# Kernel optimization log

Measured on AMD Instinct MI355X. Metric: run time of the kernel, lower is better.

Reference implementation:

```python
import jax, jax.numpy as jnp
import numpy as np

C = 256
NUM_HEADS = 4
NBLK = 6  # 3 stages x depth 2
WS = (2, 8, 8)   # 3D window
SS = (1, 4, 4)   # shift for odd blocks
N_WIN = WS[0] * WS[1] * WS[2]  # 128 tokens per window
RPB_SIZE = (2 * WS[0] - 1) * (2 * WS[1] - 1) * (2 * WS[2] - 1)  # 675


def _rel_index():
    coords = np.stack(np.meshgrid(np.arange(WS[0]), np.arange(WS[1]), np.arange(WS[2]), indexing='ij'))
    coords = coords.reshape(3, -1)
    rel = (coords[:, :, None] - coords[:, None, :]).transpose(1, 2, 0)
    rel[:, :, 0] += WS[0] - 1
    rel[:, :, 1] += WS[1] - 1
    rel[:, :, 2] += WS[2] - 1
    rel[:, :, 0] *= (2 * WS[1] - 1) * (2 * WS[2] - 1)
    rel[:, :, 1] *= (2 * WS[2] - 1)
    return jnp.asarray(rel.sum(-1))  # [N_WIN, N_WIN]

REL_IDX = _rel_index()


def window_partition(x):
    # [B,D,H,W,C] -> [B*nW, N_WIN, C]
    B, D, H, W, Cc = x.shape
    x = x.reshape(B, D // WS[0], WS[0], H // WS[1], WS[1], W // WS[2], WS[2], Cc)
    return x.transpose(0, 1, 3, 5, 2, 4, 6, 7).reshape(-1, N_WIN, Cc)


def window_reverse(win, B, D, H, W):
    Cc = win.shape[-1]
    x = win.reshape(B, D // WS[0], H // WS[1], W // WS[2], WS[0], WS[1], WS[2], Cc)
    return x.transpose(0, 1, 4, 2, 5, 3, 6, 7).reshape(B, D, H, W, Cc)


def attn_mask(D, H, W):
    # standard shifted-window mask, computed on host constants
    img = np.zeros((1, D, H, W, 1), np.float32)
    cnt = 0
    for d in (slice(0, -WS[0]), slice(-WS[0], -SS[0]), slice(-SS[0], None)):
        for h in (slice(0, -WS[1]), slice(-WS[1], -SS[1]), slice(-SS[1], None)):
            for w in (slice(0, -WS[2]), slice(-WS[2], -SS[2]), slice(-SS[2], None)):
                img[:, d, h, w, :] = cnt
                cnt += 1
    mw = img.reshape(1, D // WS[0], WS[0], H // WS[1], WS[1], W // WS[2], WS[2], 1)
    mw = mw.transpose(0, 1, 3, 5, 2, 4, 6, 7).reshape(-1, N_WIN)
    diff = mw[:, None, :] - mw[:, :, None]
    return jnp.asarray(np.where(diff != 0, -100.0, 0.0).astype(np.float32))  # [nW,N,N]


def layer_norm(x, g, b):
    mu = x.mean(-1, keepdims=True)
    var = ((x - mu) ** 2).mean(-1, keepdims=True)
    return (x - mu) * jax.lax.rsqrt(var + 1e-5) * g + b


def setup_inputs() -> dict:
    key = jax.random.key(0)
    ks = jax.random.split(key, 10)
    f = jax.random.normal
    s = 0.02
    return dict(
        x=f(ks[0], (2, 2, 2, 4096, C), jnp.float32),
        n1w=jnp.ones((NBLK, C), jnp.float32), n1b=jnp.zeros((NBLK, C), jnp.float32),
        qkv_w=f(ks[1], (NBLK, C, 3 * C), jnp.float32) * s, qkv_b=jnp.zeros((NBLK, 3 * C), jnp.float32),
        rpb=f(ks[2], (NBLK, RPB_SIZE, NUM_HEADS), jnp.float32) * s,
        proj_w=f(ks[3], (NBLK, C, C), jnp.float32) * s, proj_b=jnp.zeros((NBLK, C), jnp.float32),
        n2w=jnp.ones((NBLK, C), jnp.float32), n2b=jnp.zeros((NBLK, C), jnp.float32),
        mlp1_w=f(ks[4], (NBLK, C, 4 * C), jnp.float32) * s, mlp1_b=jnp.zeros((NBLK, 4 * C), jnp.float32),
        mlp2_w=f(ks[5], (NBLK, 4 * C, C), jnp.float32) * s, mlp2_b=jnp.zeros((NBLK, C), jnp.float32),
        exp_v_w=f(ks[6], (C, 2 * C), jnp.float32) * s,
        exp_v_nw=jnp.ones((C,), jnp.float32), exp_v_nb=jnp.zeros((C,), jnp.float32),
        exp_t_w=f(ks[7], (C, 2 * C), jnp.float32) * s,
        exp_t_nw=jnp.ones((C,), jnp.float32), exp_t_nb=jnp.zeros((C,), jnp.float32),
    )


def reference(x, n1w, n1b, qkv_w, qkv_b, rpb, proj_w, proj_b, n2w, n2b,
              mlp1_w, mlp1_b, mlp2_w, mlp2_b,
              exp_v_w, exp_v_nw, exp_v_nb, exp_t_w, exp_t_nw, exp_t_nb):
    B, T, V, L, _ = x.shape
    H = W = int(round(np.sqrt(L)))
    NH = NUM_HEADS
    dh = C // NH

    def block(h, i, D, shifted, mask):
        # h: [B, D, L, C]
        sc = h
        y = layer_norm(h, n1w[i], n1b[i]).reshape(B, D, H, W, C)
        if shifted:
            y = jnp.roll(y, (-SS[0], -SS[1], -SS[2]), axis=(1, 2, 3))
        win = window_partition(y)  # [B*nW, N, C]
        qkv = (win @ qkv_w[i] + qkv_b[i]).reshape(-1, N_WIN, 3, NH, dh)
        q, k, v = jnp.moveaxis(qkv, 2, 0)              # [B*nW, N, NH, dh]
        q = q.transpose(0, 2, 1, 3)
        k = k.transpose(0, 2, 1, 3)
        v = v.transpose(0, 2, 1, 3)                     # [B*nW, NH, N, dh]
        attn = jnp.einsum('whqd,whkd->whqk', q, k) * (dh ** -0.5)
        attn = attn + rpb[i][REL_IDX].transpose(2, 0, 1)[None]
        if mask is not None:
            nW = mask.shape[0]
            attn = attn.reshape(B, nW, NH, N_WIN, N_WIN) + mask[None, :, None]
            attn = attn.reshape(-1, NH, N_WIN, N_WIN)
        attn = jax.nn.softmax(attn, axis=-1)
        out = jnp.einsum('whqk,whkd->whqd', attn, v).transpose(0, 2, 1, 3).reshape(-1, N_WIN, C)
        out = out @ proj_w[i] + proj_b[i]
        y = window_reverse(out, B, D, H, W)
        if shifted:
            y = jnp.roll(y, (SS[0], SS[1], SS[2]), axis=(1, 2, 3))
        h = sc + y.reshape(B, D, L, C)
        z = layer_norm(h, n2w[i], n2b[i])
        z = jax.nn.gelu(z @ mlp1_w[i] + mlp1_b[i], approximate=False) @ mlp2_w[i] + mlp2_b[i]
        return h + z

    def stage(h, i0, D):
        mask = attn_mask(D, H, W)
        h = block(h, i0, D, False, None)
        h = block(h, i0 + 1, D, True, mask)
        return h

    # stage 1: swin over D = T*V
    h = x.reshape(B, T * V, L, C)
    h = stage(h, 0, T * V)
    h = h.reshape(B, T, V, L, C)

    # stage 2: view patch expand (V -> 2V) + swin
    h = (h @ exp_v_w).reshape(B, T, V, L, 2, C).transpose(0, 1, 2, 4, 3, 5).reshape(B, T, 2 * V, L, C)
    h = layer_norm(h, exp_v_nw, exp_v_nb)
    V2 = 2 * V
    h = h.reshape(B, T * V2, L, C)
    h = stage(h, 2, T * V2)
    h = h.reshape(B, T, V2, L, C)

    # stage 3: temporal patch expand (T -> 2T) + swin
    h = (h @ exp_t_w).reshape(B, T, V2, L, 2, C).transpose(0, 1, 4, 2, 3, 5).reshape(B, 2 * T, V2, L, C)
    h = layer_norm(h, exp_t_nw, exp_t_nb)
    T2 = 2 * T
    h = h.reshape(B, T2 * V2, L, C)
    h = stage(h, 4, T2 * V2)
    return h.reshape(B, T2, V2, L, C)
```

## Files before the change

kernel.cpp:

```cpp
#include <hip/hip_runtime.h>

typedef __bf16 bf16x8 __attribute__((ext_vector_type(8)));
typedef float f32x4 __attribute__((ext_vector_type(4)));
typedef unsigned short u16;
typedef unsigned int u32;

__device__ __forceinline__ u16 f2b(float f) {
    union { float f; u32 u; } v; v.f = f;
    u32 r = v.u + 0x7fffu + ((v.u >> 16) & 1u);
    return (u16)(r >> 16);
}
__device__ __forceinline__ float b2f(u16 u) {
    union { u32 u; float f; } v; v.u = ((u32)u) << 16; return v.f;
}

__global__ __launch_bounds__(256) void ln_kernel(
    const float* __restrict__ h, u16* __restrict__ out,
    const float* __restrict__ g, const float* __restrict__ bb,
    int D, int dsh, int shifted, int mode)
{
    const int lane = threadIdx.x & 63;
    const int t = blockIdx.x * 4 + (threadIdx.x >> 6);
    const float4 xv = *(const float4*)(h + (size_t)t * 256 + lane * 4);
    float s = xv.x + xv.y + xv.z + xv.w;
    float s2 = xv.x*xv.x + xv.y*xv.y + xv.z*xv.z + xv.w*xv.w;
    #pragma unroll
    for (int o = 32; o > 0; o >>= 1) { s += __shfl_xor(s, o); s2 += __shfl_xor(s2, o); }
    const float mu = s * 0.00390625f;
    const float var = s2 * 0.00390625f - mu * mu;
    const float rs = 1.0f / sqrtf(var + 1e-5f);
    const int c0 = lane * 4;
    const float4 gv = *(const float4*)(g + c0);
    const float4 bv = *(const float4*)(bb + c0);
    ushort4 o4;
    o4.x = f2b((xv.x - mu) * rs * gv.x + bv.x);
    o4.y = f2b((xv.y - mu) * rs * gv.y + bv.y);
    o4.z = f2b((xv.z - mu) * rs * gv.z + bv.z);
    o4.w = f2b((xv.w - mu) * rs * gv.w + bv.w);
    size_t oidx;
    if (mode == 1) {
        oidx = (size_t)t * 256 + c0;
    } else {
        const int b = t >> (dsh + 12);
        const int rem = t & ((1 << (dsh + 12)) - 1);
        int d = rem >> 12;
        const int l = rem & 4095;
        int hh = l >> 6, ww = l & 63;
        if (shifted) { d = d ? d - 1 : D - 1; hh = (hh - 4) & 63; ww = (ww - 4) & 63; }
        const int widx = (b << (dsh + 5)) + ((d >> 1) << 6) + ((hh >> 3) << 3) + (ww >> 3);
        const int n = ((d & 1) << 6) + ((hh & 7) << 3) + (ww & 7);
        oidx = ((size_t)(widx * 128 + n)) * 256 + c0;
    }
    *(ushort4*)(out + oidx) = o4;
}

__global__ __launch_bounds__(256) void cast_kernel(const float* __restrict__ in, u16* __restrict__ out, int n4)
{
    const int i = blockIdx.x * 256 + threadIdx.x;
    if (i >= n4) return;
    const float4 v = ((const float4*)in)[i];
    ushort4 o; o.x = f2b(v.x); o.y = f2b(v.y); o.z = f2b(v.z); o.w = f2b(v.w);
    ((ushort4*)out)[i] = o;
}

__global__ __launch_bounds__(256) void wt_kernel(const float* __restrict__ src, u16* __restrict__ dst, int K, int N)
{
    const size_t base = (size_t)blockIdx.y * K * N;
    const int idx = blockIdx.x * 256 + threadIdx.x;
    const int k = idx / N, n = idx - k * N;
    dst[base + (size_t)n * K + k] = f2b(src[base + idx]);
}

struct GemmP {
    const u16* A; const u16* Bt;
    int K;
    const float* bias;
    u16* outb;
    float* outf;
    const float* hin; float* hout;
    int D, shifted, nwsh, row_off;
};

template <int EPI>
__global__ __launch_bounds__(256, 2) void gemm_kernel(GemmP p)
{
    __shared__ __align__(16) u16 As[128 * 40];
    __shared__ __align__(16) u16 Bs[128 * 40];
    const int tid = threadIdx.x;
    const int m0 = blockIdx.x * 128, n0 = blockIdx.y * 128;
    const int K = p.K;
    f32x4 acc[4][4];
    #pragma unroll
    for (int a = 0; a < 4; a++)
        #pragma unroll
        for (int b = 0; b < 4; b++)
            acc[a][b] = f32x4{0.f, 0.f, 0.f, 0.f};

    const int r0 = tid >> 2;
    const int c8 = (tid & 3) * 8;
    const u16* Ag = p.A + (size_t)m0 * K;
    const u16* Bg = p.Bt + (size_t)n0 * K;
    const int lane = tid & 63;
    const int wv = tid >> 6;
    const int wm = (wv & 1) * 64, wn = (wv >> 1) * 64;
    const int l16 = lane & 15, quad = lane >> 4;

    for (int k0 = 0; k0 < K; k0 += 32) {
        const uint4 a0 = *(const uint4*)(Ag + (size_t)r0 * K + k0 + c8);
        const uint4 a1 = *(const uint4*)(Ag + (size_t)(r0 + 64) * K + k0 + c8);
        const uint4 b0 = *(const uint4*)(Bg + (size_t)r0 * K + k0 + c8);
        const uint4 b1 = *(const uint4*)(Bg + (size_t)(r0 + 64) * K + k0 + c8);
        __syncthreads();
        *(uint4*)(As + r0 * 40 + c8) = a0;
        *(uint4*)(As + (r0 + 64) * 40 + c8) = a1;
        *(uint4*)(Bs + r0 * 40 + c8) = b0;
        *(uint4*)(Bs + (r0 + 64) * 40 + c8) = b1;
        __syncthreads();
        bf16x8 af[4], bfr[4];
        #pragma unroll
        for (int mt = 0; mt < 4; mt++) af[mt] = *(const bf16x8*)(As + (wm + mt * 16 + l16) * 40 + quad * 8);
        #pragma unroll
        for (int nt = 0; nt < 4; nt++) bfr[nt] = *(const bf16x8*)(Bs + (wn + nt * 16 + l16) * 40 + quad * 8);
        #pragma unroll
        for (int mt = 0; mt < 4; mt++)
            #pragma unroll
            for (int nt = 0; nt < 4; nt++)
                acc[mt][nt] = __builtin_amdgcn_mfma_f32_16x16x32_bf16(af[mt], bfr[nt], acc[mt][nt], 0, 0, 0);
    }

    #pragma unroll
    for (int mt = 0; mt < 4; mt++) {
        #pragma unroll
        for (int nt = 0; nt < 4; nt++) {
            #pragma unroll
            for (int i = 0; i < 4; i++) {
                const int row = m0 + wm + mt * 16 + quad * 4 + i;
                const int col = n0 + wn + nt * 16 + l16;
                float v = acc[mt][nt][i];
                if constexpr (EPI == 0) {
                    v += p.bias[col];
                    if (col < 256) v *= 0.125f;
                    p.outb[(size_t)row * 768 + col] = f2b(v);
                } else if constexpr (EPI == 1) {
                    v += p.bias[col];
                    const int widx = row >> 7, n = row & 127;
                    const int b = widx >> p.nwsh, rem = widx & ((1 << p.nwsh) - 1);
                    int dd = ((rem >> 6) << 1) + (n >> 6);
                    int hh = (((rem >> 3) & 7) << 3) + ((n >> 3) & 7);
                    int ww = ((rem & 7) << 3) + (n & 7);
                    if (p.shifted) { dd = (dd + 1 == p.D) ? 0 : dd + 1; hh = (hh + 4) & 63; ww = (ww + 4) & 63; }
                    const size_t idx = ((size_t)((b * p.D + dd) * 4096 + hh * 64 + ww)) * 256 + col;
                    p.hout[idx] = p.hin[idx] + v;
                } else if constexpr (EPI == 2) {
                    v += p.bias[col];
                    v = 0.5f * v * (1.0f + erff(v * 0.7071067811865475f));
                    p.outb[(size_t)row * 1024 + col] = f2b(v);
                } else if constexpr (EPI == 3) {
                    v += p.bias[col];
                    const size_t idx = (size_t)(p.row_off + row) * 256 + col;
                    p.hout[idx] = p.hin[idx] + v;
                } else {
                    p.outf[(size_t)row * 512 + col] = v;
                }
            }
        }
    }
}

__global__ __launch_bounds__(256, 2) void attn_mfma_kernel(
    const u16* __restrict__ qkv, u16* __restrict__ att,
    const float* __restrict__ rpbp, int D, int shifted, int w0g, int nwsh)
{
    __shared__ __align__(16) char smem[57856];
    u16* Qs = (u16*)smem;
    u16* Ks = (u16*)(smem + 18432);
    u16* Ps = (u16*)smem;
    u16* Vt = (u16*)(smem + 36864);
    float* rb = (float*)(smem + 54272);
    int* lbl = (int*)(smem + 56972);

    const int wloc = blockIdx.x;
    const int head = blockIdx.y;
    const int tid = threadIdx.x;
    const u16* base = qkv + (size_t)wloc * 98304;

    #pragma unroll
    for (int it = 0; it < 4; it++) {
        const int id = it * 256 + tid;
        const int row = id >> 3, oct = id & 7;
        const size_t ro = (size_t)row * 768 + head * 64 + oct * 8;
        *(uint4*)(Qs + row * 72 + oct * 8) = *(const uint4*)(base + ro);
        *(uint4*)(Ks + row * 72 + oct * 8) = *(const uint4*)(base + ro + 256);
        uint4 vv = *(const uint4*)(base + ro + 512);
        const u16* vp = (const u16*)&vv;
        #pragma unroll
        for (int q = 0; q < 8; q++) Vt[(oct * 8 + q) * 136 + row] = vp[q];
    }
    for (int j = tid; j < 675; j += 256) rb[j] = rpbp[j * 4 + head];
    if (tid < 128) {
        int lv = 0;
        if (shifted) {
            const int widx = w0g + wloc;
            const int rem = widx & ((1 << nwsh) - 1);
            const int d0 = rem >> 6, h0 = (rem >> 3) & 7, w0 = rem & 7;
            const int wd = tid >> 6, wh = (tid >> 3) & 7, ww = tid & 7;
            const int rd = (d0 < (D >> 1) - 1) ? 0 : (1 + wd);
            const int rh = (h0 < 7) ? 0 : (1 + (wh >= 4));
            const int rw = (w0 < 7) ? 0 : (1 + (ww >= 4));
            lv = rd * 9 + rh * 3 + rw;
        }
        lbl[tid] = lv;
    }
    __syncthreads();

    const int wq = tid >> 6;
    const int lane = tid & 63;
    const int l16 = lane & 15, quad = lane >> 4;
    const int myrow0 = wq * 32;

    f32x4 sc[2][8];
    #pragma unroll
    for (int mt = 0; mt < 2; mt++)
        #pragma unroll
        for (int nt = 0; nt < 8; nt++)
            sc[mt][nt] = f32x4{0.f, 0.f, 0.f, 0.f};
    #pragma unroll
    for (int kt = 0; kt < 2; kt++) {
        bf16x8 aq[2];
        #pragma unroll
        for (int mt = 0; mt < 2; mt++)
            aq[mt] = *(const bf16x8*)(Qs + (myrow0 + mt * 16 + l16) * 72 + kt * 32 + quad * 8);
        bf16x8 bk[8];
        #pragma unroll
        for (int nt = 0; nt < 8; nt++)
            bk[nt] = *(const bf16x8*)(Ks + (nt * 16 + l16) * 72 + kt * 32 + quad * 8);
        #pragma unroll
        for (int mt = 0; mt < 2; mt++)
            #pragma unroll
            for (int nt = 0; nt < 8; nt++)
                sc[mt][nt] = __builtin_amdgcn_mfma_f32_16x16x32_bf16(aq[mt], bk[nt], sc[mt][nt], 0, 0, 0);
    }

    float linv[2][4];
    #pragma unroll
    for (int mt = 0; mt < 2; mt++) {
        #pragma unroll
        for (int i = 0; i < 4; i++) {
            const int row = myrow0 + mt * 16 + quad * 4 + i;
            const int rbase = ((row >> 6) + 1) * 225 + (((row >> 3) & 7) + 7) * 15 + ((row & 7) + 7);
            const int lq = lbl[row];
            float mx = -1e30f;
            float sv[8];
            #pragma unroll
            for (int nt = 0; nt < 8; nt++) {
                const int col = nt * 16 + l16;
                float v = sc[mt][nt][i] + rb[rbase - (col >> 6) * 225 - ((col >> 3) & 7) * 15 - (col & 7)];
                if (shifted && lq != lbl[col]) v -= 100.0f;
                sv[nt] = v;
                mx = fmaxf(mx, v);
            }
            #pragma unroll
            for (int o = 1; o < 16; o <<= 1) mx = fmaxf(mx, __shfl_xor(mx, o));
            float l = 0.0f;
            #pragma unroll
            for (int nt = 0; nt < 8; nt++) {
                const float pp = __expf(sv[nt] - mx);
                sc[mt][nt][i] = pp;
                l += pp;
            }
            #pragma unroll
            for (int o = 1; o < 16; o <<= 1) l += __shfl_xor(l, o);
            linv[mt][i] = 1.0f / l;
        }
    }

    __syncthreads();
    #pragma unroll
    for (int mt = 0; mt < 2; mt++)
        #pragma unroll
        for (int nt = 0; nt < 8; nt++)
            #pragma unroll
            for (int i = 0; i < 4; i++)
                Ps[(myrow0 + mt * 16 + quad * 4 + i) * 136 + nt * 16 + l16] = f2b(sc[mt][nt][i]);

    f32x4 oc[2][4];
    #pragma unroll
    for (int mt = 0; mt < 2; mt++)
        #pragma unroll
        for (int nt = 0; nt < 4; nt++)
            oc[mt][nt] = f32x4{0.f, 0.f, 0.f, 0.f};
    #pragma unroll
    for (int kt = 0; kt < 4; kt++) {
        bf16x8 ap[2];
        #pragma unroll
        for (int mt = 0; mt < 2; mt++)
            ap[mt] = *(const bf16x8*)(Ps + (myrow0 + mt * 16 + l16) * 136 + kt * 32 + quad * 8);
        bf16x8 bv[4];
        #pragma unroll
        for (int nt = 0; nt < 4; nt++)
            bv[nt] = *(const bf16x8*)(Vt + (nt * 16 + l16) * 136 + kt * 32 + quad * 8);
        #pragma unroll
        for (int mt = 0; mt < 2; mt++)
            #pragma unroll
            for (int nt = 0; nt < 4; nt++)
                oc[mt][nt] = __builtin_amdgcn_mfma_f32_16x16x32_bf16(ap[mt], bv[nt], oc[mt][nt], 0, 0, 0);
    }

    #pragma unroll
    for (int mt = 0; mt < 2; mt++)
        #pragma unroll
        for (int nt = 0; nt < 4; nt++)
            #pragma unroll
            for (int i = 0; i < 4; i++) {
                const int row = myrow0 + mt * 16 + quad * 4 + i;
                const int col = nt * 16 + l16;
                att[(size_t)(wloc * 128 + row) * 256 + head * 64 + col] = f2b(oc[mt][nt][i] * linv[mt][i]);
            }
}

__global__ __launch_bounds__(256) void expand_ln_kernel(
    const float* __restrict__ sc, float* __restrict__ hout,
    const float* __restrict__ g, const float* __restrict__ bb,
    int it0, int typ)
{
    const int lane = threadIdx.x & 63;
    const int ot = blockIdx.x * 4 + (threadIdx.x >> 6);
    const int itl = ot >> 1, e = ot & 1;
    const float4 xv = *(const float4*)(sc + (size_t)itl * 512 + e * 256 + lane * 4);
    float s = xv.x + xv.y + xv.z + xv.w;
    float s2 = xv.x*xv.x + xv.y*xv.y + xv.z*xv.z + xv.w*xv.w;
    #pragma unroll
    for (int o = 32; o > 0; o >>= 1) { s += __shfl_xor(s, o); s2 += __shfl_xor(s2, o); }
    const float mu = s * 0.00390625f;
    const float var = s2 * 0.00390625f - mu * mu;
    const float rs = 1.0f / sqrtf(var + 1e-5f);
    const int c0 = lane * 4;
    const float4 gv = *(const float4*)(g + c0);
    const float4 bv = *(const float4*)(bb + c0);
    float4 y;
    y.x = (xv.x - mu) * rs * gv.x + bv.x;
    y.y = (xv.y - mu) * rs * gv.y + bv.y;
    y.z = (xv.z - mu) * rs * gv.z + bv.z;
    y.w = (xv.w - mu) * rs * gv.w + bv.w;
    const int it = it0 + itl;
    size_t otg;
    if (typ == 0) {
        const int b = it >> 14, rr = it & 16383;
        const int t = rr >> 13, v = (rr >> 12) & 1, l = rr & 4095;
        otg = (size_t)(((b * 2 + t) * 4 + v * 2 + e) * 4096 + l);
    } else {
        const int b = it >> 15, rr = it & 32767;
        const int t = rr >> 14, v2 = (rr >> 12) & 3, l = rr & 4095;
        otg = (size_t)(((b * 4 + t * 2 + e) * 4 + v2) * 4096 + l);
    }
    *(float4*)(hout + otg * 256 + c0) = y;
}

extern "C" void kernel_launch(void* const* d_in, const int* in_sizes, int n_in,
                              void* d_out, int out_size, void* d_ws, size_t ws_size,
                              hipStream_t stream)
{
    const float* x      = (const float*)d_in[0];
    const float* n1w    = (const float*)d_in[1];
    const float* n1b    = (const float*)d_in[2];
    const float* qkv_w  = (const float*)d_in[3];
    const float* qkv_b  = (const float*)d_in[4];
    const float* rpb    = (const float*)d_in[5];
    const float* proj_w = (const float*)d_in[6];
    const float* proj_b = (const float*)d_in[7];
    const float* n2w    = (const float*)d_in[8];
    const float* n2b    = (const float*)d_in[9];
    const float* mlp1_w = (const float*)d_in[10];
    const float* mlp1_b = (const float*)d_in[11];
    const float* mlp2_w = (const float*)d_in[12];
    const float* mlp2_b = (const float*)d_in[13];
    const float* expv_w = (const float*)d_in[14];
    const float* expv_nw= (const float*)d_in[15];
    const float* expv_nb= (const float*)d_in[16];
    const float* expt_w = (const float*)d_in[17];
    const float* expt_nw= (const float*)d_in[18];
    const float* expt_nb= (const float*)d_in[19];
    (void)in_sizes; (void)n_in; (void)out_size;

    if (ws_size < 352321536ULL) return;

    char* ws = (char*)d_ws;
    float* h    = (float*)ws;
    u16*  winb  = (u16*)(ws + 134217728LL);
    u16*  att   = (u16*)(ws + 134217728LL + 67108864LL);
    char* scr   = ws + 134217728LL + 2LL * 67108864LL;
    u16*  scrb  = (u16*)scr;
    float* scrf = (float*)scr;
    u16* qkvT   = (u16*)(ws + 134217728LL + 3LL * 67108864LL);
    u16* projT  = qkvT + 6 * 768 * 256;
    u16* mlp1T  = projT + 6 * 256 * 256;
    u16* mlp2T  = mlp1T + 6 * 1024 * 256;
    u16* expvT  = mlp2T + 6 * 256 * 1024;
    u16* exptT  = expvT + 512 * 256;

    wt_kernel<<<dim3(768, 6), 256, 0, stream>>>(qkv_w, qkvT, 256, 768);
    wt_kernel<<<dim3(256, 6), 256, 0, stream>>>(proj_w, projT, 256, 256);
    wt_kernel<<<dim3(1024, 6), 256, 0, stream>>>(mlp1_w, mlp1T, 256, 1024);
    wt_kernel<<<dim3(1024, 6), 256, 0, stream>>>(mlp2_w, mlp2T, 1024, 256);
    wt_kernel<<<dim3(512, 1), 256, 0, stream>>>(expv_w, expvT, 256, 512);
    wt_kernel<<<dim3(512, 1), 256, 0, stream>>>(expt_w, exptT, 256, 512);
    hipMemcpyAsync(h, x, 33554432ULL, hipMemcpyDeviceToDevice, stream);

    for (int s = 0; s < 3; s++) {
        const int D = 4 << s;
        const int dsh = 2 + s;
        const int nwsh = dsh + 5;
        const int tokens = 2 * D * 4096;
        const int nch = tokens / 32768;
        for (int j = 0; j < 2; j++) {
            const int i = 2 * s + j;
            ln_kernel<<<dim3(tokens / 4), 256, 0, stream>>>(h, winb, n1w + i * 256, n1b + i * 256, D, dsh, j, 0);
            for (int c = 0; c < nch; c++) {
                GemmP gq{};
                gq.A = winb + (size_t)c * 32768 * 256;
                gq.Bt = qkvT + (size_t)i * 768 * 256;
                gq.K = 256; gq.bias = qkv_b + i * 768; gq.outb = scrb;
                gemm_kernel<0><<<dim3(256, 6), 256, 0, stream>>>(gq);
                attn_mfma_kernel<<<dim3(256, 4), 256, 0, stream>>>(scrb, att + (size_t)c * 32768 * 256,
                                                                   rpb + i * 675 * 4, D, j, c * 256, nwsh);
            }
            GemmP gp{};
            gp.A = att; gp.Bt = projT + (size_t)i * 256 * 256; gp.K = 256;
            gp.bias = proj_b + i * 256; gp.hin = h; gp.hout = h;
            gp.D = D; gp.shifted = j; gp.nwsh = nwsh;
            gemm_kernel<1><<<dim3(tokens / 128, 2), 256, 0, stream>>>(gp);
            ln_kernel<<<dim3(tokens / 4), 256, 0, stream>>>(h, winb, n2w + i * 256, n2b + i * 256, D, dsh, 0, 1);
            for (int c = 0; c < nch; c++) {
                GemmP g1{};
                g1.A = winb + (size_t)c * 32768 * 256;
                g1.Bt = mlp1T + (size_t)i * 1024 * 256;
                g1.K = 256; g1.bias = mlp1_b + i * 1024; g1.outb = scrb;
                gemm_kernel<2><<<dim3(256, 8), 256, 0, stream>>>(g1);
                GemmP g2{};
                g2.A = scrb; g2.Bt = mlp2T + (size_t)i * 256 * 1024; g2.K = 1024;
                g2.bias = mlp2_b + i * 256; g2.hin = h; g2.row_off = c * 32768;
                g2.hout = (s == 2 && j == 1) ? (float*)d_out : h;
                gemm_kernel<3><<<dim3(256, 2), 256, 0, stream>>>(g2);
            }
        }
        if (s < 2) {
            const int ntok = tokens;
            cast_kernel<<<dim3(ntok * 64 / 256), 256, 0, stream>>>(h, winb, ntok * 64);
            const u16* eT = (s == 0) ? expvT : exptT;
            const float* eg = (s == 0) ? expv_nw : expt_nw;
            const float* eb = (s == 0) ? expv_nb : expt_nb;
            for (int c = 0; c < ntok / 32768; c++) {
                GemmP ge{};
                ge.A = winb + (size_t)c * 32768 * 256; ge.Bt = eT; ge.K = 256; ge.outf = scrf;
                gemm_kernel<4><<<dim3(256, 4), 256, 0, stream>>>(ge);
                expand_ln_kernel<<<dim3(16384), 256, 0, stream>>>(scrf, h, eg, eb, c * 32768, s);
            }
        }
    }
}
```

Before: 3.006 ms.

## Use direct global-to-LDS loads with swizzle and stage GEMM epilogue through LDS

The GEMM main loop now uses global_load_lds to copy A/B tiles straight into shared memory, skipping the register round trip. Bank conflicts are avoided with an XOR swizzle instead of a padded stride. The epilogue writes accumulators to an LDS staging buffer in four 32-row chunks so each thread can issue wide vectorized global stores and residual loads instead of scattered scalar ones. This adds extra barriers per chunk and relies on the direct-to-LDS load semantics being correct.

```diff
diff --git a/kernel.cpp b/kernel.cpp
--- a/kernel.cpp
+++ b/kernel.cpp
@@ -12,6 +12,11 @@
 }
 __device__ __forceinline__ float b2f(u16 u) {
     union { u32 u; float f; } v; v.u = ((u32)u) << 16; return v.f;
+}
+__device__ __forceinline__ void gl_lds16(const u16* g, u16* l) {
+    __builtin_amdgcn_global_load_lds(
+        (const __attribute__((address_space(1))) void*)g,
+        (__attribute__((address_space(3))) void*)l, 16, 0, 0);
 }
 
 __global__ __launch_bounds__(256) void ln_kernel(
@@ -84,43 +89,48 @@
 template <int EPI>
 __global__ __launch_bounds__(256, 2) void gemm_kernel(GemmP p)
 {
-    __shared__ __align__(16) u16 As[128 * 40];
-    __shared__ __align__(16) u16 Bs[128 * 40];
+    __shared__ __align__(16) char smem[16896];
+    u16* As = (u16*)smem;
+    u16* Bs = (u16*)(smem + 8192);
+    float* CF = (float*)smem;
+
     const int tid = threadIdx.x;
     const int m0 = blockIdx.x * 128, n0 = blockIdx.y * 128;
     const int K = p.K;
-    f32x4 acc[4][4];
-    #pragma unroll
-    for (int a = 0; a < 4; a++)
-        #pragma unroll
-        for (int b = 0; b < 4; b++)
-            acc[a][b] = f32x4{0.f, 0.f, 0.f, 0.f};
-
-    const int r0 = tid >> 2;
-    const int c8 = (tid & 3) * 8;
-    const u16* Ag = p.A + (size_t)m0 * K;
-    const u16* Bg = p.Bt + (size_t)n0 * K;
     const int lane = tid & 63;
     const int wv = tid >> 6;
     const int wm = (wv & 1) * 64, wn = (wv >> 1) * 64;
     const int l16 = lane & 15, quad = lane >> 4;
 
+    f32x4 acc[4][4];
+    #pragma unroll
+    for (int a = 0; a < 4; a++)
+        #pragma unroll
+        for (int b = 0; b < 4; b++)
+            acc[a][b] = f32x4{0.f, 0.f, 0.f, 0.f};
+
+    const int lrow = lane >> 2;
+    const int c16s = (lane & 3) ^ (lrow & 3);
+    const int rA0 = wv * 16;
+    const u16* Ag = p.A + (size_t)(m0 + rA0 + lrow) * K + c16s * 8;
+    const u16* Bg = p.Bt + (size_t)(n0 + rA0 + lrow) * K + c16s * 8;
+    u16* Al = As + rA0 * 32;
+    u16* Bl = Bs + rA0 * 32;
+    const size_t j64 = (size_t)64 * K;
+    const int fslot = (quad ^ (l16 & 3)) * 8;
+
     for (int k0 = 0; k0 < K; k0 += 32) {
-        const uint4 a0 = *(const uint4*)(Ag + (size_t)r0 * K + k0 + c8);
-        const uint4 a1 = *(const uint4*)(Ag + (size_t)(r0 + 64) * K + k0 + c8);
-        const uint4 b0 = *(const uint4*)(Bg + (size_t)r0 * K + k0 + c8);
-        const uint4 b1 = *(const uint4*)(Bg + (size_t)(r0 + 64) * K + k0 + c8);
         __syncthreads();
-        *(uint4*)(As + r0 * 40 + c8) = a0;
-        *(uint4*)(As + (r0 + 64) * 40 + c8) = a1;
-        *(uint4*)(Bs + r0 * 40 + c8) = b0;
-        *(uint4*)(Bs + (r0 + 64) * 40 + c8) = b1;
+        gl_lds16(Ag + k0, Al);
+        gl_lds16(Ag + j64 + k0, Al + 64 * 32);
+        gl_lds16(Bg + k0, Bl);
+        gl_lds16(Bg + j64 + k0, Bl + 64 * 32);
         __syncthreads();
         bf16x8 af[4], bfr[4];
         #pragma unroll
-        for (int mt = 0; mt < 4; mt++) af[mt] = *(const bf16x8*)(As + (wm + mt * 16 + l16) * 40 + quad * 8);
-        #pragma unroll
-        for (int nt = 0; nt < 4; nt++) bfr[nt] = *(const bf16x8*)(Bs + (wn + nt * 16 + l16) * 40 + quad * 8);
+        for (int mt = 0; mt < 4; mt++) af[mt] = *(const bf16x8*)(As + (wm + mt * 16 + l16) * 32 + fslot);
+        #pragma unroll
+        for (int nt = 0; nt < 4; nt++) bfr[nt] = *(const bf16x8*)(Bs + (wn + nt * 16 + l16) * 32 + fslot);
         #pragma unroll
         for (int mt = 0; mt < 4; mt++)
             #pragma unroll
@@ -128,41 +138,91 @@
                 acc[mt][nt] = __builtin_amdgcn_mfma_f32_16x16x32_bf16(af[mt], bfr[nt], acc[mt][nt], 0, 0, 0);
     }
 
-    #pragma unroll
-    for (int mt = 0; mt < 4; mt++) {
-        #pragma unroll
-        for (int nt = 0; nt < 4; nt++) {
-            #pragma unroll
-            for (int i = 0; i < 4; i++) {
-                const int row = m0 + wm + mt * 16 + quad * 4 + i;
-                const int col = n0 + wn + nt * 16 + l16;
-                float v = acc[mt][nt][i];
-                if constexpr (EPI == 0) {
-                    v += p.bias[col];
-                    if (col < 256) v *= 0.125f;
-                    p.outb[(size_t)row * 768 + col] = f2b(v);
-                } else if constexpr (EPI == 1) {
-                    v += p.bias[col];
-                    const int widx = row >> 7, n = row & 127;
-                    const int b = widx >> p.nwsh, rem = widx & ((1 << p.nwsh) - 1);
-                    int dd = ((rem >> 6) << 1) + (n >> 6);
-                    int hh = (((rem >> 3) & 7) << 3) + ((n >> 3) & 7);
-                    int ww = ((rem & 7) << 3) + (n & 7);
-                    if (p.shifted) { dd = (dd + 1 == p.D) ? 0 : dd + 1; hh = (hh + 4) & 63; ww = (ww + 4) & 63; }
-                    const size_t idx = ((size_t)((b * p.D + dd) * 4096 + hh * 64 + ww)) * 256 + col;
-                    p.hout[idx] = p.hin[idx] + v;
-                } else if constexpr (EPI == 2) {
-                    v += p.bias[col];
-                    v = 0.5f * v * (1.0f + erff(v * 0.7071067811865475f));
-                    p.outb[(size_t)row * 1024 + col] = f2b(v);
-                } else if constexpr (EPI == 3) {
-                    v += p.bias[col];
-                    const size_t idx = (size_t)(p.row_off + row) * 256 + col;
-                    p.hout[idx] = p.hin[idx] + v;
-                } else {
-                    p.outf[(size_t)row * 512 + col] = v;
-                }
-            }
+    const int crow = tid >> 3;
+    const int ccol = (tid & 7) * 16;
+    #pragma unroll
+    for (int c = 0; c < 4; c++) {
+        __syncthreads();
+        if ((wv & 1) == (c >> 1)) {
+            const int mt0 = (c & 1) * 2;
+            #pragma unroll
+            for (int mt2 = 0; mt2 < 2; mt2++)
+                #pragma unroll
+                for (int nt = 0; nt < 4; nt++)
+                    #pragma unroll
+                    for (int i = 0; i < 4; i++)
+                        CF[(mt2 * 16 + quad * 4 + i) * 132 + wn + nt * 16 + l16] = acc[mt0 + mt2][nt][i];
+        }
+        __syncthreads();
+        const int rowg = m0 + c * 32 + crow;
+        const int colg = n0 + ccol;
+        float v[16];
+        #pragma unroll
+        for (int j = 0; j < 16; j += 4) {
+            const float4 t = *(const float4*)(CF + crow * 132 + ccol + j);
+            v[j] = t.x; v[j+1] = t.y; v[j+2] = t.z; v[j+3] = t.w;
+        }
+        if constexpr (EPI == 0) {
+            union { u16 s[16]; uint4 q[2]; } pk;
+            #pragma unroll
+            for (int j = 0; j < 16; j++) {
+                float t = v[j] + p.bias[colg + j];
+                if (colg + j < 256) t *= 0.125f;
+                pk.s[j] = f2b(t);
+            }
+            u16* op = p.outb + (size_t)rowg * 768 + colg;
+            *(uint4*)op = pk.q[0];
+            *(uint4*)(op + 8) = pk.q[1];
+        } else if constexpr (EPI == 1) {
+            const int widx = rowg >> 7, n = rowg & 127;
+            const int b = widx >> p.nwsh, rem = widx & ((1 << p.nwsh) - 1);
+            int dd = ((rem >> 6) << 1) + (n >> 6);
+            int hh = (((rem >> 3) & 7) << 3) + ((n >> 3) & 7);
+            int ww = ((rem & 7) << 3) + (n & 7);
+            if (p.shifted) { dd = (dd + 1 == p.D) ? 0 : dd + 1; hh = (hh + 4) & 63; ww = (ww + 4) & 63; }
+            const size_t tok = (size_t)((b * p.D + dd) * 4096 + hh * 64 + ww);
+            const float* hi = p.hin + tok * 256 + colg;
+            float* ho = p.hout + tok * 256 + colg;
+            #pragma unroll
+            for (int j = 0; j < 16; j += 4) {
+                const float4 r = *(const float4*)(hi + j);
+                float4 o;
+                o.x = r.x + v[j]   + p.bias[colg + j];
+                o.y = r.y + v[j+1] + p.bias[colg + j + 1];
+                o.z = r.z + v[j+2] + p.bias[colg + j + 2];
+                o.w = r.w + v[j+3] + p.bias[colg + j + 3];
+                *(float4*)(ho + j) = o;
+            }
+        } else if constexpr (EPI == 2) {
+            union { u16 s[16]; uint4 q[2]; } pk;
+            #pragma unroll
+            for (int j = 0; j < 16; j++) {
+                float t = v[j] + p.bias[colg + j];
+                t = 0.5f * t * (1.0f + erff(t * 0.7071067811865475f));
+                pk.s[j] = f2b(t);
+            }
+            u16* op = p.outb + (size_t)rowg * 1024 + colg;
+            *(uint4*)op = pk.q[0];
+            *(uint4*)(op + 8) = pk.q[1];
+        } else if constexpr (EPI == 3) {
+            const size_t tok = (size_t)(p.row_off + rowg);
+            const float* hi = p.hin + tok * 256 + colg;
+            float* ho = p.hout + tok * 256 + colg;
+            #pragma unroll
+            for (int j = 0; j < 16; j += 4) {
+                const float4 r = *(const float4*)(hi + j);
+                float4 o;
+                o.x = r.x + v[j]   + p.bias[colg + j];
+                o.y = r.y + v[j+1] + p.bias[colg + j + 1];
+                o.z = r.z + v[j+2] + p.bias[colg + j + 2];
+                o.w = r.w + v[j+3] + p.bias[colg + j + 3];
+                *(float4*)(ho + j) = o;
+            }
+        } else {
+            float* op = p.outf + (size_t)rowg * 512 + colg;
+            #pragma unroll
+            for (int j = 0; j < 16; j += 4)
+                *(float4*)(op + j) = float4{v[j], v[j+1], v[j+2], v[j+3]};
         }
     }
 }
```

After: 3.163 ms. 5.2% more time.

## Double-buffer GEMM tiles with direct global-to-LDS loads and staged epilogue

Applied to the files above, without the earlier changes.

Moves GEMM operand loads to direct global-to-LDS transfers into a double-buffered, XOR-swizzled shared tile, so the load of the next K-slice overlaps the MFMA work on the current one and each iteration needs one barrier instead of two. The epilogue now stages accumulators through shared memory, letting each thread handle contiguous float4 groups of columns for bias, residual and GELU with vectorized stores. In exchange it uses more LDS and adds barriers in the epilogue, and it relies on the async LDS loads completing before the following barrier.

```diff
diff --git a/kernel.cpp b/kernel.cpp
--- a/kernel.cpp
+++ b/kernel.cpp
@@ -12,6 +12,11 @@
 }
 __device__ __forceinline__ float b2f(u16 u) {
     union { u32 u; float f; } v; v.u = ((u32)u) << 16; return v.f;
+}
+__device__ __forceinline__ void gl_lds16(const u16* g, u16* l) {
+    __builtin_amdgcn_global_load_lds(
+        (const __attribute__((address_space(1))) void*)g,
+        (__attribute__((address_space(3))) void*)l, 16, 0, 0);
 }
 
 __global__ __launch_bounds__(256) void ln_kernel(
@@ -84,84 +89,131 @@
 template <int EPI>
 __global__ __launch_bounds__(256, 2) void gemm_kernel(GemmP p)
 {
-    __shared__ __align__(16) u16 As[128 * 40];
-    __shared__ __align__(16) u16 Bs[128 * 40];
+    __shared__ __align__(16) char smem[33792];
+    float* CF = (float*)smem;
+
     const int tid = threadIdx.x;
     const int m0 = blockIdx.x * 128, n0 = blockIdx.y * 128;
     const int K = p.K;
-    f32x4 acc[4][4];
-    #pragma unroll
-    for (int a = 0; a < 4; a++)
-        #pragma unroll
-        for (int b = 0; b < 4; b++)
-            acc[a][b] = f32x4{0.f, 0.f, 0.f, 0.f};
-
-    const int r0 = tid >> 2;
-    const int c8 = (tid & 3) * 8;
-    const u16* Ag = p.A + (size_t)m0 * K;
-    const u16* Bg = p.Bt + (size_t)n0 * K;
     const int lane = tid & 63;
     const int wv = tid >> 6;
     const int wm = (wv & 1) * 64, wn = (wv >> 1) * 64;
     const int l16 = lane & 15, quad = lane >> 4;
 
-    for (int k0 = 0; k0 < K; k0 += 32) {
-        const uint4 a0 = *(const uint4*)(Ag + (size_t)r0 * K + k0 + c8);
-        const uint4 a1 = *(const uint4*)(Ag + (size_t)(r0 + 64) * K + k0 + c8);
-        const uint4 b0 = *(const uint4*)(Bg + (size_t)r0 * K + k0 + c8);
-        const uint4 b1 = *(const uint4*)(Bg + (size_t)(r0 + 64) * K + k0 + c8);
-        __syncthreads();
-        *(uint4*)(As + r0 * 40 + c8) = a0;
-        *(uint4*)(As + (r0 + 64) * 40 + c8) = a1;
-        *(uint4*)(Bs + r0 * 40 + c8) = b0;
-        *(uint4*)(Bs + (r0 + 64) * 40 + c8) = b1;
-        __syncthreads();
+    f32x4 acc[4][4];
+    #pragma unroll
+    for (int a = 0; a < 4; a++)
+        #pragma unroll
+        for (int b = 0; b < 4; b++)
+            acc[a][b] = f32x4{0.f, 0.f, 0.f, 0.f};
+
+    const int lrow = lane >> 2;
+    const int c16s = (lane & 3) ^ (lrow & 3);
+    const int rA0 = wv * 16;
+    const u16* Ag = p.A + (size_t)(m0 + rA0 + lrow) * K + c16s * 8;
+    const u16* Bg = p.Bt + (size_t)(n0 + rA0 + lrow) * K + c16s * 8;
+    const size_t j64 = (size_t)64 * K;
+    const int fslot = (quad ^ (l16 & 3)) * 8;
+
+    {
+        u16* Al = (u16*)smem + rA0 * 32;
+        u16* Bl = (u16*)(smem + 8192) + rA0 * 32;
+        gl_lds16(Ag, Al);
+        gl_lds16(Ag + j64, Al + 64 * 32);
+        gl_lds16(Bg, Bl);
+        gl_lds16(Bg + j64, Bl + 64 * 32);
+    }
+    __syncthreads();
+
+    int kb = 0;
+    for (int k0 = 0; k0 < K; k0 += 32, kb ^= 1) {
+        if (k0 + 32 < K) {
+            char* nb = smem + (kb ^ 1) * 16384;
+            u16* Al = (u16*)nb + rA0 * 32;
+            u16* Bl = (u16*)(nb + 8192) + rA0 * 32;
+            gl_lds16(Ag + k0 + 32, Al);
+            gl_lds16(Ag + j64 + k0 + 32, Al + 64 * 32);
+            gl_lds16(Bg + k0 + 32, Bl);
+            gl_lds16(Bg + j64 + k0 + 32, Bl + 64 * 32);
+        }
+        const u16* As = (const u16*)(smem + kb * 16384);
+        const u16* Bs = (const u16*)(smem + kb * 16384 + 8192);
         bf16x8 af[4], bfr[4];
         #pragma unroll
-        for (int mt = 0; mt < 4; mt++) af[mt] = *(const bf16x8*)(As + (wm + mt * 16 + l16) * 40 + quad * 8);
-        #pragma unroll
-        for (int nt = 0; nt < 4; nt++) bfr[nt] = *(const bf16x8*)(Bs + (wn + nt * 16 + l16) * 40 + quad * 8);
+        for (int mt = 0; mt < 4; mt++) af[mt] = *(const bf16x8*)(As + (wm + mt * 16 + l16) * 32 + fslot);
+        #pragma unroll
+        for (int nt = 0; nt < 4; nt++) bfr[nt] = *(const bf16x8*)(Bs + (wn + nt * 16 + l16) * 32 + fslot);
         #pragma unroll
         for (int mt = 0; mt < 4; mt++)
             #pragma unroll
             for (int nt = 0; nt < 4; nt++)
                 acc[mt][nt] = __builtin_amdgcn_mfma_f32_16x16x32_bf16(af[mt], bfr[nt], acc[mt][nt], 0, 0, 0);
-    }
-
-    #pragma unroll
-    for (int mt = 0; mt < 4; mt++) {
-        #pragma unroll
-        for (int nt = 0; nt < 4; nt++) {
-            #pragma unroll
-            for (int i = 0; i < 4; i++) {
-                const int row = m0 + wm + mt * 16 + quad * 4 + i;
-                const int col = n0 + wn + nt * 16 + l16;
-                float v = acc[mt][nt][i];
-                if constexpr (EPI == 0) {
-                    v += p.bias[col];
-                    if (col < 256) v *= 0.125f;
-                    p.outb[(size_t)row * 768 + col] = f2b(v);
-                } else if constexpr (EPI == 1) {
-                    v += p.bias[col];
-                    const int widx = row >> 7, n = row & 127;
-                    const int b = widx >> p.nwsh, rem = widx & ((1 << p.nwsh) - 1);
-                    int dd = ((rem >> 6) << 1) + (n >> 6);
-                    int hh = (((rem >> 3) & 7) << 3) + ((n >> 3) & 7);
-                    int ww = ((rem & 7) << 3) + (n & 7);
-                    if (p.shifted) { dd = (dd + 1 == p.D) ? 0 : dd + 1; hh = (hh + 4) & 63; ww = (ww + 4) & 63; }
-                    const size_t idx = ((size_t)((b * p.D + dd) * 4096 + hh * 64 + ww)) * 256 + col;
-                    p.hout[idx] = p.hin[idx] + v;
-                } else if constexpr (EPI == 2) {
-                    v += p.bias[col];
-                    v = 0.5f * v * (1.0f + erff(v * 0.7071067811865475f));
-                    p.outb[(size_t)row * 1024 + col] = f2b(v);
-                } else if constexpr (EPI == 3) {
-                    v += p.bias[col];
-                    const size_t idx = (size_t)(p.row_off + row) * 256 + col;
-                    p.hout[idx] = p.hin[idx] + v;
-                } else {
-                    p.outf[(size_t)row * 512 + col] = v;
-                }
+        __syncthreads();
+    }
+
+    const int crow = tid >> 2;
+    const int p4 = (tid & 3) * 4;
+    #pragma unroll
+    for (int c = 0; c < 2; c++) {
+        if (c) __syncthreads();
+        if ((wv & 1) == c) {
+            #pragma unroll
+            for (int mt = 0; mt < 4; mt++)
+                #pragma unroll
+                for (int nt = 0; nt < 4; nt++)
+                    #pragma unroll
+                    for (int i = 0; i < 4; i++)
+                        CF[(mt * 16 + quad * 4 + i) * 132 + wn + nt * 16 + l16] = acc[mt][nt][i];
+        }
+        __syncthreads();
+        const int rowg = m0 + c * 64 + crow;
+        size_t tokbase = 0;
+        if constexpr (EPI == 1) {
+            const int widx = rowg >> 7, n = rowg & 127;
+            const int b = widx >> p.nwsh, rem = widx & ((1 << p.nwsh) - 1);
+            int dd = ((rem >> 6) << 1) + (n >> 6);
+            int hh = (((rem >> 3) & 7) << 3) + ((n >> 3) & 7);
+            int ww = ((rem & 7) << 3) + (n & 7);
+            if (p.shifted) { dd = (dd + 1 == p.D) ? 0 : dd + 1; hh = (hh + 4) & 63; ww = (ww + 4) & 63; }
+            tokbase = ((size_t)((b * p.D + dd) * 4096 + hh * 64 + ww)) * 256;
+        } else if constexpr (EPI == 3) {
+            tokbase = (size_t)(p.row_off + rowg) * 256;
+        }
+        #pragma unroll
+        for (int j = 0; j < 8; j++) {
+            const int colf = j * 16 + p4;
+            const int colg = n0 + colf;
+            const float4 t = *(const float4*)(CF + crow * 132 + colf);
+            const float4 bi = (EPI <= 3) ? *(const float4*)(p.bias + colg) : float4{0.f,0.f,0.f,0.f};
+            if constexpr (EPI == 0) {
+                const float sc = (colg < 256) ? 0.125f : 1.0f;
+                ushort4 pk;
+                pk.x = f2b((t.x + bi.x) * sc);
+                pk.y = f2b((t.y + bi.y) * sc);
+                pk.z = f2b((t.z + bi.z) * sc);
+                pk.w = f2b((t.w + bi.w) * sc);
+                *(ushort4*)(p.outb + (size_t)rowg * 768 + colg) = pk;
+            } else if constexpr (EPI == 1 || EPI == 3) {
+                const float* hi = p.hin + tokbase + colg;
+                float* ho = p.hout + tokbase + colg;
+                const float4 r = *(const float4*)hi;
+                float4 o;
+                o.x = r.x + t.x + bi.x;
+                o.y = r.y + t.y + bi.y;
+                o.z = r.z + t.z + bi.z;
+                o.w = r.w + t.w + bi.w;
+                *(float4*)ho = o;
+            } else if constexpr (EPI == 2) {
+                float4 g4;
+                g4.x = t.x + bi.x; g4.y = t.y + bi.y; g4.z = t.z + bi.z; g4.w = t.w + bi.w;
+                ushort4 pk;
+                pk.x = f2b(0.5f * g4.x * (1.0f + erff(g4.x * 0.7071067811865475f)));
+                pk.y = f2b(0.5f * g4.y * (1.0f + erff(g4.y * 0.7071067811865475f)));
+                pk.z = f2b(0.5f * g4.z * (1.0f + erff(g4.z * 0.7071067811865475f)));
+                pk.w = f2b(0.5f * g4.w * (1.0f + erff(g4.w * 0.7071067811865475f)));
+                *(ushort4*)(p.outb + (size_t)rowg * 1024 + colg) = pk;
+            } else {
+                *(float4*)(p.outf + (size_t)rowg * 512 + colg) = t;
             }
         }
     }
```

New measurement: 2.769 ms. 1.09x faster.
